# Optimization experiments

Measured on AMD Instinct MI355X. Metric: run time of the kernel, lower is better.

Reference implementation:

```python
import jax, jax.numpy as jnp
import numpy as np

B, T, L, D = 4, 32, 64, 768
NHEAD, DFF, NLAYERS, NSPK = 12, 2048, 2, 4
DH = D // NHEAD


def setup_inputs() -> dict:
    key = jax.random.key(0)
    ks = jax.random.split(key, 12)
    s = 0.02
    return {
        "token_embeddings": jax.random.normal(ks[0], (B, T, L, D), jnp.float32) * s,
        "speaker_ids": jax.random.randint(ks[1], (B, T), 0, NSPK, jnp.int32),
        "Wq": jax.random.normal(ks[2], (D, D), jnp.float32) * s,
        "Wk": jax.random.normal(ks[3], (D, D), jnp.float32) * s,
        "Wv": jax.random.normal(ks[4], (D, D), jnp.float32) * s,
        "in_proj_w": jax.random.normal(ks[5], (NLAYERS, 3 * D, D), jnp.float32) * s,
        "in_proj_b": jnp.zeros((NLAYERS, 3 * D), jnp.float32),
        "out_w": jax.random.normal(ks[6], (NLAYERS, D, D), jnp.float32) * s,
        "out_b": jnp.zeros((NLAYERS, D), jnp.float32),
        "ln1_g": jnp.ones((NLAYERS, D), jnp.float32),
        "ln1_b": jnp.zeros((NLAYERS, D), jnp.float32),
        "ff1_w": jax.random.normal(ks[7], (NLAYERS, DFF, D), jnp.float32) * s,
        "ff1_b": jnp.zeros((NLAYERS, DFF), jnp.float32),
        "ff2_w": jax.random.normal(ks[8], (NLAYERS, D, DFF), jnp.float32) * s,
        "ff2_b": jnp.zeros((NLAYERS, D), jnp.float32),
        "ln2_g": jnp.ones((NLAYERS, D), jnp.float32),
        "ln2_b": jnp.zeros((NLAYERS, D), jnp.float32),
    }


def _layer_norm(x, g, b, eps=1e-5):
    mu = x.mean(-1, keepdims=True)
    var = ((x - mu) ** 2).mean(-1, keepdims=True)
    return (x - mu) * jax.lax.rsqrt(var + eps) * g + b


def _mha(x, w_in, b_in, w_out, b_out):
    # x: (N, L, D); torch nn.MultiheadAttention with in_proj/out_proj
    N, Lx, _ = x.shape
    qkv = x @ w_in.T + b_in  # (N, L, 3D)
    q, k, v = jnp.split(qkv, 3, axis=-1)
    def heads(z):
        return z.reshape(N, Lx, NHEAD, DH).transpose(0, 2, 1, 3)  # (N,H,L,dh)
    q, k, v = heads(q), heads(k), heads(v)
    scores = jnp.einsum("nhqd,nhkd->nhqk", q, k) / jnp.sqrt(jnp.float32(DH))
    attn = jax.nn.softmax(scores, axis=-1)
    out = jnp.einsum("nhqk,nhkd->nhqd", attn, v)
    out = out.transpose(0, 2, 1, 3).reshape(N, Lx, D)
    return out @ w_out.T + b_out


def reference(token_embeddings, speaker_ids, Wq, Wk, Wv, in_proj_w, in_proj_b,
              out_w, out_b, ln1_g, ln1_b, ff1_w, ff1_b, ff2_w, ff2_b, ln2_g, ln2_b):
    # edu embeddings: mean over token dim (frozen-BERT output stand-in)
    edu = token_embeddings.mean(axis=2)              # (B,T,D)
    tok = token_embeddings @ Wq.T                    # query_proj on tokens (B,T,L,D)
    k = edu @ Wk.T                                   # (B,T,D)
    v = edu @ Wv.T                                   # (B,T,D)
    # SAUTE: per-speaker causal cumulative sum of outer products k_u v_u^T
    same_spk = speaker_ids[:, :, None] == speaker_ids[:, None, :]
    causal = jnp.arange(T)[None, :, None] >= jnp.arange(T)[None, None, :]
    maskf = (same_spk & causal).astype(k.dtype)      # (B,T,T)
    M = jnp.einsum("btu,bui,buj->btij", maskf, k, v)  # (B,T,D,D) speaker state
    ctx = tok + jnp.einsum("btij,btlj->btli", M, tok)  # (B,T,L,D)
    # stacked post-norm TransformerEncoder (torch defaults: ReLU, dff=2048)
    x = ctx.reshape(B * T, L, D)
    for l in range(NLAYERS):
        a = _mha(x, in_proj_w[l], in_proj_b[l], out_w[l], out_b[l])
        x = _layer_norm(x + a, ln1_g[l], ln1_b[l])
        f = jax.nn.relu(x @ ff1_w[l].T + ff1_b[l]) @ ff2_w[l].T + ff2_b[l]
        x = _layer_norm(x + f, ln2_g[l], ln2_b[l])
    return x.reshape(B, T, L, D)
```

## Files before the change

### kernel.cpp

```cpp
#include <hip/hip_runtime.h>
#include <hip/hip_bf16.h>

#define BB 4
#define TT 32
#define LL 64
#define DD 768
#define NHEAD 12
#define DH 64
#define DFF 2048
#define NLAYERS 2
#define ROWS (BB*TT*LL)
#define BTN  (BB*TT)

typedef __attribute__((ext_vector_type(8))) short bf16x8;
typedef __attribute__((ext_vector_type(4))) float f32x4;

__device__ __forceinline__ int swz64(int r, int c) {
    return r * 64 + ((c ^ (r & 7)) << 3);
}

__device__ __forceinline__ int xcd_swizzle(int orig, int nwg) {
    const int q8 = nwg >> 3, r8 = nwg & 7;
    const int xcd = orig & 7, idx = orig >> 3;
    return (xcd < r8 ? xcd * (q8 + 1) : r8 * (q8 + 1) + (xcd - r8) * q8) + idx;
}

__device__ __forceinline__ unsigned pack_bf16(float a, float b) {
    __hip_bfloat16 h0 = __float2bfloat16(a);
    __hip_bfloat16 h1 = __float2bfloat16(b);
    return (unsigned)*reinterpret_cast<unsigned short*>(&h0) |
           ((unsigned)*reinterpret_cast<unsigned short*>(&h1) << 16);
}

__device__ __forceinline__ short bf16s(float a) {
    __hip_bfloat16 h = __float2bfloat16(a);
    return *reinterpret_cast<short*>(&h);
}

struct CastArgs {
    const float* src[7];
    __hip_bfloat16* dst[7];
    int end[7];
};
__global__ __launch_bounds__(256) void cast_multi_kernel(CastArgs a)
{
    int q = blockIdx.x * 256 + threadIdx.x;
    if (q >= a.end[6]) return;
    int s = 0;
    while (q >= a.end[s]) ++s;
    int local = q - (s ? a.end[s - 1] : 0);
    float4 v = reinterpret_cast<const float4*>(a.src[s])[local];
    ushort4 o;
    __hip_bfloat16 h0 = __float2bfloat16(v.x);
    __hip_bfloat16 h1 = __float2bfloat16(v.y);
    __hip_bfloat16 h2 = __float2bfloat16(v.z);
    __hip_bfloat16 h3 = __float2bfloat16(v.w);
    o.x = *reinterpret_cast<unsigned short*>(&h0);
    o.y = *reinterpret_cast<unsigned short*>(&h1);
    o.z = *reinterpret_cast<unsigned short*>(&h2);
    o.w = *reinterpret_cast<unsigned short*>(&h3);
    reinterpret_cast<ushort4*>(a.dst[s])[local] = o;
}

__global__ __launch_bounds__(256) void te_prep_kernel(
    const float* __restrict__ te, __hip_bfloat16* __restrict__ teb,
    __hip_bfloat16* __restrict__ edu_b)
{
    int idx = blockIdx.x * 256 + threadIdx.x;
    int bt = idx / DD;
    int d  = idx - bt * DD;
    const float* p = te + ((size_t)bt * LL) * DD + d;
    __hip_bfloat16* q = teb + ((size_t)bt * LL) * DD + d;
    float s = 0.f;
#pragma unroll
    for (int l = 0; l < LL; ++l) {
        float v = p[(size_t)l * DD];
        s += v;
        q[(size_t)l * DD] = __float2bfloat16(v);
    }
    edu_b[idx] = __float2bfloat16(s * (1.0f / (float)LL));
}

template<int OUT_BF16, int RELU, int QKV>
__global__ __launch_bounds__(256) void gemm_bf16_kernel(
    const __hip_bfloat16* __restrict__ A,
    const __hip_bfloat16* __restrict__ B,
    const float* __restrict__ bias,
    void* __restrict__ Cout,
    __hip_bfloat16* __restrict__ Vout,
    int M, int N, int K, int ldC)
{
    __shared__ short lA[2][8192];
    __shared__ short lB[2][8192];
    const int tid  = threadIdx.x;
    const int lane = tid & 63;
    const int w    = tid >> 6;
    const int wr   = w >> 1, wc = w & 1;

    const int nbx = gridDim.x;
    const int wg = xcd_swizzle(blockIdx.y * nbx + blockIdx.x, nbx * gridDim.y);
    const int bm = (wg / nbx) * 128;
    const int bn = (wg % nbx) * 128;

    const int sr  = tid >> 3;
    const int cw  = tid & 7;
    const int sco = cw << 3;
    int wox[4];
#pragma unroll
    for (int i = 0; i < 4; ++i)
        wox[i] = swz64(sr + 32 * i, cw);

    const int lo = lane & 15, hi = lane >> 4;
    int roA[2][4], roB[2][4];
#pragma unroll
    for (int ks = 0; ks < 2; ++ks) {
#pragma unroll
        for (int m = 0; m < 4; ++m)
            roA[ks][m] = swz64(wr * 64 + m * 16 + lo, ks * 4 + hi);
#pragma unroll
        for (int n = 0; n < 4; ++n)
            roB[ks][n] = swz64(wc * 64 + n * 16 + lo, ks * 4 + hi);
    }

    const short* Ag = reinterpret_cast<const short*>(A);
    const short* Bg = reinterpret_cast<const short*>(B);

    f32x4 acc[4][4] = {};

    bf16x8 ra[4], rb[4];
#pragma unroll
    for (int i = 0; i < 4; ++i) {
        ra[i] = *reinterpret_cast<const bf16x8*>(Ag + (size_t)(bm + sr + 32 * i) * K + sco);
        rb[i] = *reinterpret_cast<const bf16x8*>(Bg + (size_t)(bn + sr + 32 * i) * K + sco);
    }
#pragma unroll
    for (int i = 0; i < 4; ++i) {
        *reinterpret_cast<bf16x8*>(&lA[0][wox[i]]) = ra[i];
        *reinterpret_cast<bf16x8*>(&lB[0][wox[i]]) = rb[i];
    }
    __syncthreads();

    const int NT = K >> 6;
    int cur = 0;
    for (int t = 0; t < NT; ++t) {
        const bool nx = (t + 1 < NT);
        if (nx) {
            const int kn = (t + 1) << 6;
#pragma unroll
            for (int i = 0; i < 4; ++i) {
                ra[i] = *reinterpret_cast<const bf16x8*>(Ag + (size_t)(bm + sr + 32 * i) * K + kn + sco);
                rb[i] = *reinterpret_cast<const bf16x8*>(Bg + (size_t)(bn + sr + 32 * i) * K + kn + sco);
            }
        }

#pragma unroll
        for (int ks = 0; ks < 2; ++ks) {
            bf16x8 af[4], bfr[4];
#pragma unroll
            for (int m = 0; m < 4; ++m)
                af[m] = *reinterpret_cast<const bf16x8*>(&lA[cur][roA[ks][m]]);
#pragma unroll
            for (int n = 0; n < 4; ++n)
                bfr[n] = *reinterpret_cast<const bf16x8*>(&lB[cur][roB[ks][n]]);
#pragma unroll
            for (int m = 0; m < 4; ++m)
#pragma unroll
                for (int n = 0; n < 4; ++n)
                    acc[m][n] = __builtin_amdgcn_mfma_f32_16x16x32_bf16(
                        af[m], bfr[n], acc[m][n], 0, 0, 0);
        }

        if (nx) {
#pragma unroll
            for (int i = 0; i < 4; ++i) {
                *reinterpret_cast<bf16x8*>(&lA[cur ^ 1][wox[i]]) = ra[i];
                *reinterpret_cast<bf16x8*>(&lB[cur ^ 1][wox[i]]) = rb[i];
            }
        }
        __syncthreads();
        cur ^= 1;
    }

    const int crow = (lane >> 4) * 4;
    const int ccol = lane & 15;
#pragma unroll
    for (int n = 0; n < 4; ++n) {
        const int col = bn + wc * 64 + n * 16 + ccol;
        const float bv = bias ? bias[col] : 0.f;
        if (QKV && col >= 1536) {
            const int hh = (col - 1536) >> 6;
            const int d  = (col - 1536) & 63;
#pragma unroll
            for (int m = 0; m < 4; ++m) {
                const int row0 = bm + wr * 64 + m * 16 + crow;
#pragma unroll
                for (int j = 0; j < 4; ++j) {
                    const int row = row0 + j;
                    const int ni = row >> 6, ll = row & 63;
                    Vout[(((size_t)ni * NHEAD + hh) << 12) + (d << 6) + ll] =
                        __float2bfloat16(acc[m][n][j] + bv);
                }
            }
        } else {
#pragma unroll
            for (int m = 0; m < 4; ++m) {
                const int row0 = bm + wr * 64 + m * 16 + crow;
#pragma unroll
                for (int j = 0; j < 4; ++j) {
                    float v = acc[m][n][j] + bv;
                    if (RELU) v = fmaxf(v, 0.f);
                    if (OUT_BF16)
                        reinterpret_cast<__hip_bfloat16*>(Cout)[(size_t)(row0 + j) * ldC + col] =
                            __float2bfloat16(v);
                    else
                        reinterpret_cast<float*>(Cout)[(size_t)(row0 + j) * ldC + col] = v;
                }
            }
        }
    }
}

__global__ __launch_bounds__(64) void attn_mfma_kernel(
    const __hip_bfloat16* __restrict__ qk,
    const __hip_bfloat16* __restrict__ vt,
    __hip_bfloat16* __restrict__ out)
{
    const int n = blockIdx.x, h = blockIdx.y;
    const int lane = threadIdx.x;
    const int lo = lane & 15, hi = lane >> 4;
    __shared__ short pl[64 * 72];

    const short* qg = reinterpret_cast<const short*>(qk) + (size_t)(n * 64) * 1536 + h * 64;

    f32x4 acc[4][4] = {};
#pragma unroll
    for (int ks = 0; ks < 2; ++ks) {
        const int kc = ks * 32 + hi * 8;
        bf16x8 af[4], bk[4];
#pragma unroll
        for (int m = 0; m < 4; ++m)
            af[m] = *reinterpret_cast<const bf16x8*>(qg + (size_t)(m * 16 + lo) * 1536 + kc);
#pragma unroll
        for (int nn = 0; nn < 4; ++nn)
            bk[nn] = *reinterpret_cast<const bf16x8*>(qg + 768 + (size_t)(nn * 16 + lo) * 1536 + kc);
#pragma unroll
        for (int m = 0; m < 4; ++m)
#pragma unroll
            for (int nn = 0; nn < 4; ++nn)
                acc[m][nn] = __builtin_amdgcn_mfma_f32_16x16x32_bf16(
                    af[m], bk[nn], acc[m][nn], 0, 0, 0);
    }

#pragma unroll
    for (int m = 0; m < 4; ++m) {
#pragma unroll
        for (int j = 0; j < 4; ++j) {
            float s0 = acc[m][0][j] * 0.125f;
            float s1 = acc[m][1][j] * 0.125f;
            float s2 = acc[m][2][j] * 0.125f;
            float s3 = acc[m][3][j] * 0.125f;
            float mx = fmaxf(fmaxf(s0, s1), fmaxf(s2, s3));
            mx = fmaxf(mx, __shfl_xor(mx, 1));
            mx = fmaxf(mx, __shfl_xor(mx, 2));
            mx = fmaxf(mx, __shfl_xor(mx, 4));
            mx = fmaxf(mx, __shfl_xor(mx, 8));
            float e0 = __expf(s0 - mx), e1 = __expf(s1 - mx);
            float e2 = __expf(s2 - mx), e3 = __expf(s3 - mx);
            float sm = e0 + e1 + e2 + e3;
            sm += __shfl_xor(sm, 1);
            sm += __shfl_xor(sm, 2);
            sm += __shfl_xor(sm, 4);
            sm += __shfl_xor(sm, 8);
            const float inv = 1.0f / sm;
            short* pr = &pl[(m * 16 + hi * 4 + j) * 72 + lo];
            pr[0]  = bf16s(e0 * inv);
            pr[16] = bf16s(e1 * inv);
            pr[32] = bf16s(e2 * inv);
            pr[48] = bf16s(e3 * inv);
        }
    }
    __syncthreads();

    const short* vg = reinterpret_cast<const short*>(vt) + ((size_t)(n * NHEAD + h) << 12);
    f32x4 o[4][4] = {};
#pragma unroll
    for (int ks = 0; ks < 2; ++ks) {
        const int kc = ks * 32 + hi * 8;
        bf16x8 pa[4], bv[4];
#pragma unroll
        for (int m = 0; m < 4; ++m)
            pa[m] = *reinterpret_cast<const bf16x8*>(&pl[(m * 16 + lo) * 72 + kc]);
#pragma unroll
        for (int nn = 0; nn < 4; ++nn)
            bv[nn] = *reinterpret_cast<const bf16x8*>(vg + (nn * 16 + lo) * 64 + kc);
#pragma unroll
        for (int m = 0; m < 4; ++m)
#pragma unroll
            for (int nn = 0; nn < 4; ++nn)
                o[m][nn] = __builtin_amdgcn_mfma_f32_16x16x32_bf16(
                    pa[m], bv[nn], o[m][nn], 0, 0, 0);
    }

#pragma unroll
    for (int m = 0; m < 4; ++m)
#pragma unroll
        for (int nn = 0; nn < 4; ++nn)
#pragma unroll
            for (int j = 0; j < 4; ++j)
                out[(size_t)(n * 64 + m * 16 + hi * 4 + j) * DD + h * 64 + nn * 16 + lo] =
                    __float2bfloat16(o[m][nn][j]);
}

__global__ __launch_bounds__(64) void saute_p_mfma_kernel(
    const __hip_bfloat16* __restrict__ Xb,
    const __hip_bfloat16* __restrict__ KV,
    const int* __restrict__ spk,
    __hip_bfloat16* __restrict__ P)
{
    const int lane = threadIdx.x;
    const int lo = lane & 15, hi = lane >> 4;
    const int row0 = blockIdx.x * 64;
    const int bt = row0 >> 6;
    const int b  = bt >> 5, t = bt & 31;

    const short* Ag = reinterpret_cast<const short*>(Xb) + (size_t)row0 * DD;
    const short* Bg = reinterpret_cast<const short*>(KV) + (size_t)(b * TT) * 1536 + 768;

    f32x4 acc[4][2] = {};
    for (int ks = 0; ks < 24; ++ks) {
        const int kc = ks * 32 + hi * 8;
        bf16x8 af[4], bv[2];
#pragma unroll
        for (int m = 0; m < 4; ++m)
            af[m] = *reinterpret_cast<const bf16x8*>(Ag + (size_t)(m * 16 + lo) * DD + kc);
#pragma unroll
        for (int nn = 0; nn < 2; ++nn)
            bv[nn] = *reinterpret_cast<const bf16x8*>(Bg + (size_t)(nn * 16 + lo) * 1536 + kc);
#pragma unroll
        for (int m = 0; m < 4; ++m)
#pragma unroll
            for (int nn = 0; nn < 2; ++nn)
                acc[m][nn] = __builtin_amdgcn_mfma_f32_16x16x32_bf16(
                    af[m], bv[nn], acc[m][nn], 0, 0, 0);
    }

    const int st = spk[bt];
#pragma unroll
    for (int nn = 0; nn < 2; ++nn) {
        const int u = nn * 16 + lo;
        const bool mk = (u <= t) && (spk[b * TT + u] == st);
#pragma unroll
        for (int m = 0; m < 4; ++m)
#pragma unroll
            for (int j = 0; j < 4; ++j) {
                const int row = row0 + m * 16 + hi * 4 + j;
                P[(size_t)row * 32 + u] =
                    mk ? __float2bfloat16(acc[m][nn][j]) : __float2bfloat16(0.f);
            }
    }
}

__global__ __launch_bounds__(256) void saute_ctx_kernel(
    __hip_bfloat16* __restrict__ Xb,
    const __hip_bfloat16* __restrict__ KV,
    const __hip_bfloat16* __restrict__ P)
{
    __shared__ unsigned kls[32 * 384];
    __shared__ float pls[8 * 32];
    const int row0 = blockIdx.x * 8;
    const int b = row0 >> 11;
    const int tid = threadIdx.x;

    const unsigned* k2 = reinterpret_cast<const unsigned*>(KV) + (size_t)(b * TT) * 768;
    for (int i = tid; i < 32 * 384; i += 256) {
        int u = i / 384, j = i - u * 384;
        kls[i] = k2[u * 768 + j];
    }
    pls[tid] = __bfloat162float(P[(size_t)row0 * 32 + tid]);
    __syncthreads();

    const int r = tid >> 5;
    const int l32 = tid & 31;
    unsigned* xrow = reinterpret_cast<unsigned*>(Xb + (size_t)(row0 + r) * DD);

    float2 acc[12];
#pragma unroll
    for (int c = 0; c < 12; ++c) {
        unsigned pk = xrow[l32 + 32 * c];
        acc[c].x = __uint_as_float(pk << 16);
        acc[c].y = __uint_as_float(pk & 0xffff0000u);
    }
    for (int u = 0; u < 32; ++u) {
        const float pv = pls[r * 32 + u];
        const unsigned* kr = &kls[u * 384];
#pragma unroll
        for (int c = 0; c < 12; ++c) {
            unsigned pk = kr[l32 + 32 * c];
            acc[c].x = fmaf(pv, __uint_as_float(pk << 16),          acc[c].x);
            acc[c].y = fmaf(pv, __uint_as_float(pk & 0xffff0000u), acc[c].y);
        }
    }
#pragma unroll
    for (int c = 0; c < 12; ++c)
        xrow[l32 + 32 * c] = pack_bf16(acc[c].x, acc[c].y);
}

template<int FINAL>
__global__ __launch_bounds__(192) void add_ln_kernel(
    __hip_bfloat16* __restrict__ xb, const __hip_bfloat16* __restrict__ y,
    const float* __restrict__ g, const float* __restrict__ bb,
    float* __restrict__ xf)
{
    const int row = blockIdx.x;
    const int tid = threadIdx.x;
    __shared__ float red[3];
    __shared__ float stat[2];
    const size_t base = (size_t)row * DD + tid * 4;

    uint2 xv = *reinterpret_cast<const uint2*>(xb + base);
    uint2 yv = *reinterpret_cast<const uint2*>(y + base);
    float v[4];
    v[0] = __uint_as_float(xv.x << 16)         + __uint_as_float(yv.x << 16);
    v[1] = __uint_as_float(xv.x & 0xffff0000u) + __uint_as_float(yv.x & 0xffff0000u);
    v[2] = __uint_as_float(xv.y << 16)         + __uint_as_float(yv.y << 16);
    v[3] = __uint_as_float(xv.y & 0xffff0000u) + __uint_as_float(yv.y & 0xffff0000u);

    float s = v[0] + v[1] + v[2] + v[3];
#pragma unroll
    for (int off = 32; off > 0; off >>= 1) s += __shfl_down(s, off);
    if ((tid & 63) == 0) red[tid >> 6] = s;
    __syncthreads();
    if (tid == 0) stat[0] = (red[0] + red[1] + red[2]) * (1.0f / (float)DD);
    __syncthreads();
    const float mu = stat[0];

    float d[4];
    float q = 0.f;
#pragma unroll
    for (int i = 0; i < 4; ++i) { d[i] = v[i] - mu; q += d[i] * d[i]; }
    __syncthreads();
#pragma unroll
    for (int off = 32; off > 0; off >>= 1) q += __shfl_down(q, off);
    if ((tid & 63) == 0) red[tid >> 6] = q;
    __syncthreads();
    if (tid == 0) stat[1] = (red[0] + red[1] + red[2]) * (1.0f / (float)DD);
    __syncthreads();
    const float rstd = rsqrtf(stat[1] + 1e-5f);

    float o[4];
#pragma unroll
    for (int i = 0; i < 4; ++i)
        o[i] = d[i] * rstd * g[tid * 4 + i] + bb[tid * 4 + i];

    if (FINAL) {
        float4 f4 = make_float4(o[0], o[1], o[2], o[3]);
        *reinterpret_cast<float4*>(xf + base) = f4;
    } else {
        uint2 ov;
        ov.x = pack_bf16(o[0], o[1]);
        ov.y = pack_bf16(o[2], o[3]);
        *reinterpret_cast<uint2*>(xb + base) = ov;
    }
}

extern "C" void kernel_launch(void* const* d_in, const int* in_sizes, int n_in,
                              void* d_out, int out_size, void* d_ws, size_t ws_size,
                              hipStream_t stream) {
    (void)in_sizes; (void)n_in; (void)out_size; (void)ws_size;
    const float* te  = (const float*)d_in[0];
    const int*   spk = (const int*)  d_in[1];
    const float* Wq  = (const float*)d_in[2];
    const float* Wk  = (const float*)d_in[3];
    const float* Wv  = (const float*)d_in[4];
    const float* ipw = (const float*)d_in[5];
    const float* ipb = (const float*)d_in[6];
    const float* ow  = (const float*)d_in[7];
    const float* ob  = (const float*)d_in[8];
    const float* g1  = (const float*)d_in[9];
    const float* b1  = (const float*)d_in[10];
    const float* f1w = (const float*)d_in[11];
    const float* f1b = (const float*)d_in[12];
    const float* f2w = (const float*)d_in[13];
    const float* f2b = (const float*)d_in[14];
    const float* g2  = (const float*)d_in[15];
    const float* b2  = (const float*)d_in[16];

    float* Xout = (float*)d_out;

    __hip_bfloat16* wsb   = (__hip_bfloat16*)d_ws;
    __hip_bfloat16* Wq_b  = wsb;
    __hip_bfloat16* ipw_b = Wq_b  + 589824;
    __hip_bfloat16* ow_b  = ipw_b + 3538944;
    __hip_bfloat16* f1w_b = ow_b  + 1179648;
    __hip_bfloat16* f2w_b = f1w_b + 3145728;
    __hip_bfloat16* Xb    = f2w_b + 3145728;
    __hip_bfloat16* SCR   = Xb    + 6291456;
    __hip_bfloat16* Vt    = SCR   + 12582912;
    __hip_bfloat16* Wkv_b = SCR;
    __hip_bfloat16* Ab    = SCR   + 18874368;
    __hip_bfloat16* Yb    = Ab    + 6291456;
    __hip_bfloat16* KV    = Yb    + 6291456;
    __hip_bfloat16* Pb    = KV    + 196608;
    __hip_bfloat16* edu_b = Pb    + 262144;

    te_prep_kernel<<<(BTN * DD) / 256, 256, 0, stream>>>(te, Ab, edu_b);

    CastArgs ca;
    ca.src[0] = Wq;  ca.dst[0] = Wq_b;
    ca.src[1] = ipw; ca.dst[1] = ipw_b;
    ca.src[2] = ow;  ca.dst[2] = ow_b;
    ca.src[3] = f1w; ca.dst[3] = f1w_b;
    ca.src[4] = f2w; ca.dst[4] = f2w_b;
    ca.src[5] = Wk;  ca.dst[5] = Wkv_b;
    ca.src[6] = Wv;  ca.dst[6] = Wkv_b + 589824;
    int quads[7] = {589824/4, 3538944/4, 1179648/4, 3145728/4, 3145728/4, 589824/4, 589824/4};
    int acc = 0;
    for (int i = 0; i < 7; ++i) { acc += quads[i]; ca.end[i] = acc; }
    cast_multi_kernel<<<(acc + 255) / 256, 256, 0, stream>>>(ca);

    gemm_bf16_kernel<1,0,0><<<dim3(1536/128, 1), 256, 0, stream>>>(
        edu_b, Wkv_b, nullptr, KV, nullptr, BTN, 1536, DD, 1536);

    gemm_bf16_kernel<1,0,0><<<dim3(DD/128, ROWS/128), 256, 0, stream>>>(
        Ab, Wq_b, nullptr, Xb, nullptr, ROWS, DD, DD, DD);

    saute_p_mfma_kernel<<<ROWS/64, 64, 0, stream>>>(Xb, KV, spk, Pb);
    saute_ctx_kernel<<<ROWS/8, 256, 0, stream>>>(Xb, KV, Pb);

    for (int l = 0; l < NLAYERS; ++l) {
        const __hip_bfloat16* ipw_l = ipw_b + (size_t)l * 3 * DD * DD;
        const __hip_bfloat16* ow_l  = ow_b  + (size_t)l * DD * DD;
        const __hip_bfloat16* f1w_l = f1w_b + (size_t)l * DFF * DD;
        const __hip_bfloat16* f2w_l = f2w_b + (size_t)l * DD * DFF;

        gemm_bf16_kernel<1,0,1><<<dim3(3*DD/128, ROWS/128), 256, 0, stream>>>(
            Xb, ipw_l, ipb + (size_t)l * 3 * DD, SCR, Vt, ROWS, 3*DD, DD, 1536);
        attn_mfma_kernel<<<dim3(BTN, NHEAD), 64, 0, stream>>>(SCR, Vt, Ab);
        gemm_bf16_kernel<1,0,0><<<dim3(DD/128, ROWS/128), 256, 0, stream>>>(
            Ab, ow_l, ob + (size_t)l * DD, Yb, nullptr, ROWS, DD, DD, DD);
        add_ln_kernel<0><<<ROWS, 192, 0, stream>>>(
            Xb, Yb, g1 + (size_t)l * DD, b1 + (size_t)l * DD, nullptr);
        gemm_bf16_kernel<1,1,0><<<dim3(DFF/128, ROWS/128), 256, 0, stream>>>(
            Xb, f1w_l, f1b + (size_t)l * DFF, SCR, nullptr, ROWS, DFF, DD, DFF);
        gemm_bf16_kernel<1,0,0><<<dim3(DD/128, ROWS/128), 256, 0, stream>>>(
            SCR, f2w_l, f2b + (size_t)l * DD, Yb, nullptr, ROWS, DD, DFF, DD);
        if (l == NLAYERS - 1)
            add_ln_kernel<1><<<ROWS, 192, 0, stream>>>(
                Xb, Yb, g2 + (size_t)l * DD, b2 + (size_t)l * DD, Xout);
        else
            add_ln_kernel<0><<<ROWS, 192, 0, stream>>>(
                Xb, Yb, g2 + (size_t)l * DD, b2 + (size_t)l * DD, nullptr);
    }
}
```

Baseline: 440.7 us.

## Deepen GEMM global prefetch to two tiles ahead with unrolled double-buffer loop

Restructures the bf16 MFMA GEMM main loop to unroll by two K-tiles, holding two register sets so global loads run two tiles ahead instead of one. LDS writes for the next tile are issued before the current tile's MFMAs rather than after, and row base pointers are precomputed. The aim is to hide more global memory latency behind compute. In exchange it doubles staging register use, which may reduce occupancy, and adds odd-NT edge handling.

```diff
diff --git a/kernel.cpp b/kernel.cpp
--- a/kernel.cpp
+++ b/kernel.cpp
@@ -124,44 +124,60 @@
 
     const short* Ag = reinterpret_cast<const short*>(A);
     const short* Bg = reinterpret_cast<const short*>(B);
+    const short* Arow[4];
+    const short* Brow[4];
+#pragma unroll
+    for (int i = 0; i < 4; ++i) {
+        Arow[i] = Ag + (size_t)(bm + sr + 32 * i) * K + sco;
+        Brow[i] = Bg + (size_t)(bn + sr + 32 * i) * K + sco;
+    }
 
     f32x4 acc[4][4] = {};
 
-    bf16x8 ra[4], rb[4];
+    bf16x8 raA[4], rbA[4], raB[4], rbB[4];
 #pragma unroll
     for (int i = 0; i < 4; ++i) {
-        ra[i] = *reinterpret_cast<const bf16x8*>(Ag + (size_t)(bm + sr + 32 * i) * K + sco);
-        rb[i] = *reinterpret_cast<const bf16x8*>(Bg + (size_t)(bn + sr + 32 * i) * K + sco);
+        raA[i] = *reinterpret_cast<const bf16x8*>(Arow[i]);
+        rbA[i] = *reinterpret_cast<const bf16x8*>(Brow[i]);
     }
 #pragma unroll
     for (int i = 0; i < 4; ++i) {
-        *reinterpret_cast<bf16x8*>(&lA[0][wox[i]]) = ra[i];
-        *reinterpret_cast<bf16x8*>(&lB[0][wox[i]]) = rb[i];
+        *reinterpret_cast<bf16x8*>(&lA[0][wox[i]]) = raA[i];
+        *reinterpret_cast<bf16x8*>(&lB[0][wox[i]]) = rbA[i];
+    }
+#pragma unroll
+    for (int i = 0; i < 4; ++i) {
+        raA[i] = *reinterpret_cast<const bf16x8*>(Arow[i] + 64);
+        rbA[i] = *reinterpret_cast<const bf16x8*>(Brow[i] + 64);
     }
     __syncthreads();
 
     const int NT = K >> 6;
-    int cur = 0;
-    for (int t = 0; t < NT; ++t) {
-        const bool nx = (t + 1 < NT);
-        if (nx) {
-            const int kn = (t + 1) << 6;
+    for (int t = 0; t < NT; t += 2) {
+        if (t + 2 < NT) {
+            const int kn = (t + 2) << 6;
 #pragma unroll
             for (int i = 0; i < 4; ++i) {
-                ra[i] = *reinterpret_cast<const bf16x8*>(Ag + (size_t)(bm + sr + 32 * i) * K + kn + sco);
-                rb[i] = *reinterpret_cast<const bf16x8*>(Bg + (size_t)(bn + sr + 32 * i) * K + kn + sco);
-            }
-        }
-
+                raB[i] = *reinterpret_cast<const bf16x8*>(Arow[i] + kn);
+                rbB[i] = *reinterpret_cast<const bf16x8*>(Brow[i] + kn);
+            }
+        }
+        if (t + 1 < NT) {
+#pragma unroll
+            for (int i = 0; i < 4; ++i) {
+                *reinterpret_cast<bf16x8*>(&lA[1][wox[i]]) = raA[i];
+                *reinterpret_cast<bf16x8*>(&lB[1][wox[i]]) = rbA[i];
+            }
+        }
 #pragma unroll
         for (int ks = 0; ks < 2; ++ks) {
             bf16x8 af[4], bfr[4];
 #pragma unroll
             for (int m = 0; m < 4; ++m)
-                af[m] = *reinterpret_cast<const bf16x8*>(&lA[cur][roA[ks][m]]);
+                af[m] = *reinterpret_cast<const bf16x8*>(&lA[0][roA[ks][m]]);
 #pragma unroll
             for (int n = 0; n < 4; ++n)
-                bfr[n] = *reinterpret_cast<const bf16x8*>(&lB[cur][roB[ks][n]]);
+                bfr[n] = *reinterpret_cast<const bf16x8*>(&lB[0][roB[ks][n]]);
 #pragma unroll
             for (int m = 0; m < 4; ++m)
 #pragma unroll
@@ -169,16 +185,42 @@
                     acc[m][n] = __builtin_amdgcn_mfma_f32_16x16x32_bf16(
                         af[m], bfr[n], acc[m][n], 0, 0, 0);
         }
-
-        if (nx) {
-#pragma unroll
-            for (int i = 0; i < 4; ++i) {
-                *reinterpret_cast<bf16x8*>(&lA[cur ^ 1][wox[i]]) = ra[i];
-                *reinterpret_cast<bf16x8*>(&lB[cur ^ 1][wox[i]]) = rb[i];
-            }
-        }
         __syncthreads();
-        cur ^= 1;
+
+        if (t + 1 < NT) {
+            if (t + 3 < NT) {
+                const int kn = (t + 3) << 6;
+#pragma unroll
+                for (int i = 0; i < 4; ++i) {
+                    raA[i] = *reinterpret_cast<const bf16x8*>(Arow[i] + kn);
+                    rbA[i] = *reinterpret_cast<const bf16x8*>(Brow[i] + kn);
+                }
+            }
+            if (t + 2 < NT) {
+#pragma unroll
+                for (int i = 0; i < 4; ++i) {
+                    *reinterpret_cast<bf16x8*>(&lA[0][wox[i]]) = raB[i];
+                    *reinterpret_cast<bf16x8*>(&lB[0][wox[i]]) = rbB[i];
+                }
+            }
+#pragma unroll
+            for (int ks = 0; ks < 2; ++ks) {
+                bf16x8 af[4], bfr[4];
+#pragma unroll
+                for (int m = 0; m < 4; ++m)
+                    af[m] = *reinterpret_cast<const bf16x8*>(&lA[1][roA[ks][m]]);
+#pragma unroll
+                for (int n = 0; n < 4; ++n)
+                    bfr[n] = *reinterpret_cast<const bf16x8*>(&lB[1][roB[ks][n]]);
+#pragma unroll
+                for (int m = 0; m < 4; ++m)
+#pragma unroll
+                    for (int n = 0; n < 4; ++n)
+                        acc[m][n] = __builtin_amdgcn_mfma_f32_16x16x32_bf16(
+                            af[m], bfr[n], acc[m][n], 0, 0, 0);
+            }
+            __syncthreads();
+        }
     }
 
     const int crow = (lane >> 4) * 4;
```

Measured after the change: 678.9 us. 54.0% more time.
